# Kernel optimization log

Hardware: AMD Instinct MI355X
Metric: run time of the kernel (lower is better)

## Reference

```python
import jax, jax.numpy as jnp
import numpy as np

B, N, H, NH = 8, 1024, 768, 12
AS = H // NH
SCALE = AS ** -0.5
NEG_SLOPE = 0.02  # LeakyReLU(0.02)
M = 256           # occurrence pairs per batch item


def _lin(k, out_d, in_d):
    k1, k2 = jax.random.split(k)
    w = jax.random.normal(k1, (out_d, in_d), jnp.float32) * (in_d ** -0.5)
    b = jax.random.normal(k2, (out_d,), jnp.float32) * 0.01
    return w, b


def setup_inputs():
    key = jax.random.key(0)
    ks = jax.random.split(key, 10)
    W_var, b_var = _lin(ks[0], H, H)
    W_sym, b_sym = _lin(ks[1], H, H)
    W_score, b_score = _lin(ks[2], 1, 2 * H)
    W_cross, b_cross = _lin(ks[3], 1, H)
    W_atom, b_atom = _lin(ks[4], H, 2 * H)
    W_q, b_q = _lin(ks[5], H, H)
    W_k, b_k = _lin(ks[6], H, H)
    W_v, b_v = _lin(ks[7], H, H)
    W_o, b_o = _lin(ks[8], H, H)
    x = jax.random.normal(ks[9], (B, N, H), jnp.float32)
    # predicates every 3rd node starting at 2 (no overlapping writes, i+1 < N)
    pp = np.zeros((B, N), np.int32)
    pp[:, 2:N - 2:3] = 1
    rng = np.random.default_rng(0)
    occ = np.stack([rng.permutation(N)[:2 * M].reshape(M, 2) for _ in range(B)]).astype(np.int32)
    return dict(
        x=x,
        atom_graph=jnp.zeros((B, N, N), jnp.float32),
        variable_graph=jnp.zeros((B, N, N), jnp.float32),
        W_var=W_var, b_var=b_var, W_sym=W_sym, b_sym=b_sym,
        W_score=W_score, b_score=b_score, W_cross=W_cross, b_cross=b_cross,
        W_atom=W_atom, b_atom=b_atom, W_q=W_q, b_q=b_q, W_k=W_k, b_k=b_k,
        W_v=W_v, b_v=b_v, W_o=W_o, b_o=b_o,
        predicate_pos=jnp.asarray(pp),
        variable_tags=jnp.zeros((B, N), jnp.int32),
        attention_mask=jnp.ones((B, N), jnp.int32),
        occurrence_list=jnp.asarray(occ),
    )


def reference(x, atom_graph, variable_graph,
              W_var, b_var, W_sym, b_sym, W_score, b_score, W_cross, b_cross,
              W_atom, b_atom, W_q, b_q, W_k, b_k, W_v, b_v, W_o, b_o,
              predicate_pos, variable_tags, attention_mask, occurrence_list):
    lrelu = lambda v: jax.nn.leaky_relu(v, NEG_SLOPE)
    idx = jnp.arange(N)
    pred = predicate_pos == 1                              # [B,N]
    pp_prev2 = jnp.roll(predicate_pos, 2, axis=1)          # pp[i-2]
    # branch: single-neighbor var (i==0 or pp[i-2]==1) vs averaged neighbors
    single = (idx[None, :] == 0) | ((idx[None, :] >= 2) & (pp_prev2 == 1))
    x_prev = jnp.roll(x, 1, axis=1)
    x_next = jnp.roll(x, -1, axis=1)
    var_in = jnp.where(single[..., None], x_next, (x_prev + x_next) * 0.5)
    var_feat = var_in @ W_var.T + b_var
    sym_feat = x @ W_sym.T + b_sym
    t = jnp.tanh(jnp.concatenate([var_feat, sym_feat], axis=-1))
    s = lrelu(t @ W_score.T + b_score)[..., 0]             # [B,N] edge scores
    # write masks: (i-1,i)/(i,i-1) for preds i>=1; (i,i+1)/(i+1,i) for i<=1 or double branch
    lower = pred & (idx[None, :] >= 1)
    upper = pred & ((idx[None, :] <= 1) | ~single)
    sl = jnp.where(lower, s, 0.0)
    su = jnp.where(upper, s, 0.0)
    im1 = jnp.clip(idx - 1, 0, N - 1)
    ip1 = jnp.clip(idx + 1, 0, N - 1)
    AG = atom_graph
    AG = AG.at[:, im1, idx].add(sl).at[:, idx, im1].add(sl)
    AG = AG.at[:, idx, ip1].add(su).at[:, ip1, idx].add(su)
    # variable (cross-atom occurrence) graph
    o0, o1 = occurrence_list[..., 0], occurrence_list[..., 1]
    barange = jnp.arange(B)[:, None]
    xm = (x[barange, o0] + x[barange, o1]) * 0.5           # [B,M,H]
    sc = lrelu(xm @ W_cross.T + b_cross)[..., 0]           # [B,M]
    VG = variable_graph.at[barange, o0, o1].add(sc).at[barange, o1, o0].add(sc)
    # multi-head attention with graph biases
    q = (x @ W_q.T + b_q).reshape(B, N, NH, AS).transpose(0, 2, 1, 3) * SCALE
    k = (x @ W_k.T + b_k).reshape(B, N, NH, AS).transpose(0, 2, 1, 3)
    v = (x @ W_v.T + b_v).reshape(B, N, NH, AS).transpose(0, 2, 1, 3)
    att = jnp.einsum('bhnd,bhmd->bhnm', q, k)
    AG = 0.2 * AG + 0.8 * (AG @ AG)
    VG2 = VG @ VG
    att = att + AG[:, None] + VG2[:, None]
    att = jax.nn.softmax(att, axis=-1)                     # dropout omitted (eval)
    y = jnp.einsum('bhnm,bhmd->bhnd', att, v).transpose(0, 2, 1, 3).reshape(B, N, H)
    y = y @ W_o.T + b_o
    # path embedding: weighted mean of per-predicate atom embeds (weight 2 or 3)
    y_prev = jnp.roll(y, 1, axis=1)
    y_next = jnp.roll(y, -1, axis=1)
    var_y = jnp.where(single[..., None], y_next, (y_prev + y_next) * 0.5)
    atom = jnp.concatenate([var_y, y], axis=-1) @ W_atom.T + b_atom  # [B,N,H]
    triple = upper & (idx[None, :] >= 1)
    w = jnp.where(pred, jnp.where(triple, 3.0, 2.0), 0.0)
    pm = (w[..., None] * atom).sum(axis=1) / w.sum(axis=1)[:, None]  # [B,H]
    return jnp.broadcast_to(pm[:, None, :], (B, N, H))
```

## Files before the change

kernel.cpp:

```cpp
#include <hip/hip_runtime.h>
#include <hip/hip_bf16.h>

#define BB 8
#define NN 1024
#define HH 768
#define NHD 12
#define ASZ 64
#define MM 256
#define QSCALE 0.125f
#define NSLOPE 0.02f
#define LOG2E 1.44269504f
#define PRMAX 384

typedef __attribute__((ext_vector_type(8))) short bf16x8;
typedef __attribute__((ext_vector_type(4))) float f32x4;

#define EXP2F(x) __builtin_amdgcn_exp2f(x)
#define RCPF(x)  __builtin_amdgcn_rcpf(x)

#define OFFB_QB    ((size_t)0)
#define OFFB_KB    ((size_t)12582912)
#define OFFB_VB    ((size_t)25165824)
#define OFFB_XB    ((size_t)37748736)
#define OFFB_WQB   ((size_t)50331648)
// ... 72 lines not shown
  if (lane == 0) { pcnt[b] = base; sumw[b] = wacc; }
  for (int c = lane; c < NN; c += 64) { sraw[b * NN + c] = 0.f; diag[b * NN + c] = 0.f; }
  for (int c = lane; c < HH; c += 64) {
    zz[b * HH + c] = 0.f;
    zz[BB * HH + b * HH + c] = 0.f;
  }
}

#define NXQ (BB * NN * HH / 4)
#define WQ  (HH * HH / 4)
#define NCVT ((NXQ + 5 * WQ) / 256)
__global__ void k_cvtall(const float* __restrict__ x,
                         const float* __restrict__ s1, const float* __restrict__ s2,
                         const float* __restrict__ s3, const float* __restrict__ s4,
                         const float* __restrict__ s5,
                         ushort* __restrict__ dx,
                         ushort* __restrict__ d1, ushort* __restrict__ d2,
                         ushort* __restrict__ d3, ushort* __restrict__ d4,
                         ushort* __restrict__ d5,
                         const int* __restrict__ occ, const float* __restrict__ Wc,
                         const float* __restrict__ bc, float* __restrict__ diag) {
  if (blockIdx.x < NCVT) {
    int idx = blockIdx.x * 256 + threadIdx.x;
    const float* src; ushort* dst; int off;
    if (idx < NXQ) { src = x; dst = dx; off = idx; }
    else {
      int r = idx - NXQ;
      int z = r / WQ;
      off = r - z * WQ;
      src = z == 0 ? s1 : z == 1 ? s2 : z == 2 ? s3 : z == 3 ? s4 : s5;
      dst = z == 0 ? d1 : z == 1 ? d2 : z == 2 ? d3 : z == 3 ? d4 : d5;
    }
    float4 v = ((const float4*)src)[off];
    ushort4 o;
    o.x = f2bf(v.x); o.y = f2bf(v.y); o.z = f2bf(v.z); o.w = f2bf(v.w);
    ((ushort4*)dst)[off] = o;
  } else {
    int g = (blockIdx.x - NCVT) * 4 + (threadIdx.x >> 6);
    int lane = threadIdx.x & 63;
    int b = g >> 8, m = g & (MM - 1);
    int o0 = occ[(b * MM + m) * 2 + 0];
    int o1 = occ[(b * MM + m) * 2 + 1];
    const float* x0 = x + (size_t)(b * NN + o0) * HH;
    const float* x1 = x + (size_t)(b * NN + o1) * HH;
    float acc = 0.f;
    for (int d = lane; d < HH; d += 64) acc += 0.5f * (x0[d] + x1[d]) * Wc[d];
    for (int off = 32; off; off >>= 1) acc += __shfl_xor(acc, off);
    if (lane == 0) {
      float sc = lrelu(acc + bc[0]);
      float sq = sc * sc;
      diag[b * NN + o0] = sq;
      diag[b * NN + o1] = sq;
    }
  }
}

__global__ void k_gather(const ushort* __restrict__ xb, const int* __restrict__ pp,
                         const int* __restrict__ plist, const int* __restrict__ pcnt,
                         ushort* __restrict__ vrows) {
  int b = blockIdx.y;
  int j = blockIdx.x * 4 + (threadIdx.x >> 6);
  int lane = threadIdx.x & 63;
  if (j >= pcnt[b]) return;
  int i = plist[b * NN + j];
  bool sing = (i == 0) || (i >= 2 && pp[b * NN + i - 2] == 1);
  float wa = sing ? 0.f : 0.5f, wb = sing ? 1.f : 0.5f;
  const ushort* rp = xb + (size_t)(b * NN + ((i - 1) & (NN - 1))) * HH;
  const ushort* rn = xb + (size_t)(b * NN + ((i + 1) & (NN - 1))) * HH;
  ushort* dst = vrows + ((size_t)b * PRMAX + j) * HH;
#pragma unroll
  for (int it = 0; it < 3; ++it) {
    int d4 = lane + it * 64;
    ushort4 p4 = ((const ushort4*)rp)[d4];
    ushort4 n4 = ((const ushort4*)rn)[d4];
    ushort4 o;
    o.x = f2bf(wa * bf2f(p4.x) + wb * bf2f(n4.x));
    o.y = f2bf(wa * bf2f(p4.y) + wb * bf2f(n4.y));
    o.z = f2bf(wa * bf2f(p4.z) + wb * bf2f(n4.z));
    o.w = f2bf(wa * bf2f(p4.w) + wb * bf2f(n4.w));
    ((ushort4*)dst)[d4] = o;
  }
}

__global__ __launch_bounds__(256, 2) void k_score_mf(
    const ushort* __restrict__ xb, const ushort* __restrict__ vrows,
    const int* __restrict__ plist, const int* __restrict__ pcnt,
    const ushort* __restrict__ Wvar, const ushort* __restrict__ Wsym,
    const float* __restrict__ bvar, const float* __restrict__ bsym,
    const float* __restrict__ wscore, float* __restrict__ s_raw) {
  const int b = blockIdx.z;
  const int cnt = pcnt[b];
  const int j0 = blockIdx.y * 64;
  if (j0 >= cnt) return;
  const int n0g = blockIdx.x * 128;
  const bool symh = n0g >= HH;
  const int n0 = symh ? n0g - HH : n0g;
  const ushort* W = symh ? Wsym : Wvar;
  const float* bias = symh ? bsym : bvar;
  __shared__ ushort As[64 * 64];
  __shared__ ushort Bs[128 * 64];
  __shared__ int pl[64];
  __shared__ float red[64];
  const int t = threadIdx.x;
  const int w = t >> 6, lane = t & 63, lg = lane >> 4, lm = lane & 15;
  const int wm = (w >> 1) * 32, wn = (w & 1) * 64;
  if (t < 64) {
    int j = j0 + t;
    pl[t] = (j < cnt) ? plist[b * NN + j] : 2;
    red[t] = 0.f;
  }
  __syncthreads();
  const int r0 = t >> 3, c = t & 7;
  const ushort* ap0; const ushort* ap1;
  if (symh) {
    const ushort* xbb = xb + (size_t)b * NN * HH;
    ap0 = xbb + (size_t)pl[r0] * HH + c * 8;
    ap1 = xbb + (size_t)pl[r0 + 32] * HH + c * 8;
  } else {
    const ushort* vrb = vrows + ((size_t)b * PRMAX + j0) * HH;
    ap0 = vrb + (size_t)r0 * HH + c * 8;
    ap1 = vrb + (size_t)(r0 + 32) * HH + c * 8;
  }
  const ushort* bp = W + (size_t)(n0 + r0) * HH + c * 8;
  uint4 ar0 = *(const uint4*)ap0;
  uint4 ar1 = *(const uint4*)ap1;
  uint4 br0 = *(const uint4*)bp;
  uint4 br1 = *(const uint4*)(bp + (size_t)32 * HH);
  uint4 br2 = *(const uint4*)(bp + (size_t)64 * HH);
  uint4 br3 = *(const uint4*)(bp + (size_t)96 * HH);
  f32x4 acc[2][4] = {};
  const int ssw = (c ^ (r0 & 7)) * 8;
  for (int k0 = 0; k0 < HH; k0 += 64) {
    if (k0) __syncthreads();
    *(uint4*)&As[r0 * 64 + ssw] = ar0;
    *(uint4*)&As[(r0 + 32) * 64 + ssw] = ar1;
    *(uint4*)&Bs[r0 * 64 + ssw] = br0;
    *(uint4*)&Bs[(r0 + 32) * 64 + ssw] = br1;
    *(uint4*)&Bs[(r0 + 64) * 64 + ssw] = br2;
    *(uint4*)&Bs[(r0 + 96) * 64 + ssw] = br3;
    __syncthreads();
    if (k0 + 64 < HH) {
      ap0 += 64; ap1 += 64; bp += 64;
      ar0 = *(const uint4*)ap0;
      ar1 = *(const uint4*)ap1;
      br0 = *(const uint4*)bp;
      br1 = *(const uint4*)(bp + (size_t)32 * HH);
      br2 = *(const uint4*)(bp + (size_t)64 * HH);
      br3 = *(const uint4*)(bp + (size_t)96 * HH);
    }
    bf16x8 af[2][2], bfr[4][2];
#pragma unroll
    for (int mt = 0; mt < 2; ++mt)
#pragma unroll
      for (int kt = 0; kt < 2; ++kt) {
        int row = wm + mt * 16 + lm, ch = lg + kt * 4;
        af[mt][kt] = *(bf16x8*)&As[row * 64 + ((ch ^ (row & 7)) * 8)];
      }
#pragma unroll
    for (int nt = 0; nt < 4; ++nt)
#pragma unroll
      for (int kt = 0; kt < 2; ++kt) {
        int row = wn + nt * 16 + lm, ch = lg + kt * 4;
        bfr[nt][kt] = *(bf16x8*)&Bs[row * 64 + ((ch ^ (row & 7)) * 8)];
      }
#pragma unroll
    for (int mt = 0; mt < 2; ++mt)
#pragma unroll
      for (int nt = 0; nt < 4; ++nt)
#pragma unroll
        for (int kt = 0; kt < 2; ++kt)
          acc[mt][nt] = __builtin_amdgcn_mfma_f32_16x16x32_bf16(af[mt][kt], bfr[nt][kt], acc[mt][nt], 0, 0, 0);
  }
  float bcol[4], wcol[4];
#pragma unroll
  for (int nt = 0; nt < 4; ++nt) {
    int cl = wn + nt * 16 + lm;
    bcol[nt] = bias[n0 + cl];
    wcol[nt] = wscore[n0g + cl];
  }
#pragma unroll
  for (int mt = 0; mt < 2; ++mt)
#pragma unroll
    for (int r = 0; r < 4; ++r) {
      float p = 0.f;
#pragma unroll
      for (int nt = 0; nt < 4; ++nt)
        p += fast_tanh(acc[mt][nt][r] + bcol[nt]) * wcol[nt];
      p += __shfl_xor(p, 1); p += __shfl_xor(p, 2);
      p += __shfl_xor(p, 4); p += __shfl_xor(p, 8);
      if (lm == 0) atomicAdd(&red[wm + mt * 16 + lg * 4 + r], p);
    }
  __syncthreads();
  if (t < 64) {
    int j2 = j0 + t;
    if (j2 < cnt) atomicAdd(&s_raw[b * NN + pl[t]], red[t]);
  }
}

__global__ void k_bias(const int* __restrict__ pp, const float* __restrict__ s_raw,
                       const float* __restrict__ diag, const float* __restrict__ b_score,
                       float4* __restrict__ bias4) {
  int g = blockIdx.x * 256 + threadIdx.x;
  int b = g >> 10, r = g & (NN - 1);
  const int* ppb = pp + b * NN;
  int i = -1;
  if (ppb[r] == 1) i = r;
  else if (r + 1 < NN && ppb[r + 1] == 1) i = r + 1;
  else if (r >= 1 && ppb[r - 1] == 1) i = r - 1;
  float v0 = 0.f, v1 = 0.f, v2 = 0.f; int cw = r;
  if (i >= 1 && i + 1 < NN) {
    float s = lrelu(s_raw[b * NN + i] + b_score[0]);
    float s2 = s * s;
    cw = i - 1;
    if (i == r) { v0 = 0.2f * s; v1 = 1.6f * s2; v2 = 0.2f * s; }
    else       { v0 = 0.8f * s2; v1 = 0.2f * s; v2 = 0.8f * s2; }
  }
  int slot = r - cw;
  float d = diag[g];
  if (slot == 0) v0 += d; else if (slot == 1) v1 += d; else v2 += d;
  bias4[g] = make_float4(__int_as_float(cw), v0 * LOG2E, v1 * LOG2E, v2 * LOG2E);
}

__global__ __launch_bounds__(256, 2) void k_gemm_bf(
    const ushort* __restrict__ X,
    const ushort* __restrict__ W0, const ushort* __restrict__ W1, const ushort* __restrict__ W2,
    const float* __restrict__ b0, const float* __restrict__ b1, const float* __restrict__ b2,
    ushort* __restrict__ C0, ushort* __restrict__ C1, ushort* __restrict__ C2) {
  const int z = blockIdx.z;
  const ushort* W = z == 0 ? W0 : (z == 1 ? W1 : W2);
  const float* bias = z == 0 ? b0 : (z == 1 ? b1 : b2);
  ushort* C = z == 0 ? C0 : (z == 1 ? C1 : C2);
  const float alpha = z == 0 ? QSCALE * LOG2E : 1.f;
  __shared__ ushort As[128 * 64];
  __shared__ ushort Bs[128 * 64];
  const int m0 = blockIdx.x * 128, n0 = blockIdx.y * 128;
  const int t = threadIdx.x;
  const int w = t >> 6, lane = t & 63, lg = lane >> 4, lm = lane & 15;
  const int wm = (w >> 1) * 64, wn = (w & 1) * 64;
  const int r0 = t >> 3, c = t & 7;
  const int ssw = (c ^ (r0 & 7)) * 8;
  const ushort* Xp = X + (size_t)(m0 + r0) * HH + c * 8;
  const ushort* Wp = W + (size_t)(n0 + r0) * HH + c * 8;
  uint4 xa0 = *(const uint4*)Xp;
  uint4 xa1 = *(const uint4*)(Xp + (size_t)32 * HH);
  uint4 xa2 = *(const uint4*)(Xp + (size_t)64 * HH);
  uint4 xa3 = *(const uint4*)(Xp + (size_t)96 * HH);
  uint4 wb0 = *(const uint4*)Wp;
  uint4 wb1 = *(const uint4*)(Wp + (size_t)32 * HH);
  uint4 wb2 = *(const uint4*)(Wp + (size_t)64 * HH);
  uint4 wb3 = *(const uint4*)(Wp + (size_t)96 * HH);
  f32x4 acc[4][4] = {};
  for (int k0 = 0; k0 < HH; k0 += 64) {
    if (k0) __syncthreads();
    *(uint4*)&As[r0 * 64 + ssw] = xa0;
    *(uint4*)&As[(r0 + 32) * 64 + ssw] = xa1;
    *(uint4*)&As[(r0 + 64) * 64 + ssw] = xa2;
    *(uint4*)&As[(r0 + 96) * 64 + ssw] = xa3;
    *(uint4*)&Bs[r0 * 64 + ssw] = wb0;
    *(uint4*)&Bs[(r0 + 32) * 64 + ssw] = wb1;
    *(uint4*)&Bs[(r0 + 64) * 64 + ssw] = wb2;
    *(uint4*)&Bs[(r0 + 96) * 64 + ssw] = wb3;
    __syncthreads();
    if (k0 + 64 < HH) {
      Xp += 64; Wp += 64;
      xa0 = *(const uint4*)Xp;
      xa1 = *(const uint4*)(Xp + (size_t)32 * HH);
      xa2 = *(const uint4*)(Xp + (size_t)64 * HH);
      xa3 = *(const uint4*)(Xp + (size_t)96 * HH);
      wb0 = *(const uint4*)Wp;
      wb1 = *(const uint4*)(Wp + (size_t)32 * HH);
      wb2 = *(const uint4*)(Wp + (size_t)64 * HH);
      wb3 = *(const uint4*)(Wp + (size_t)96 * HH);
    }
    bf16x8 af[4][2], bfr[4][2];
#pragma unroll
    for (int mt = 0; mt < 4; ++mt)
#pragma unroll
      for (int kt = 0; kt < 2; ++kt) {
        int row = wm + mt * 16 + lm, ch = lg + kt * 4;
        af[mt][kt] = *(bf16x8*)&As[row * 64 + ((ch ^ (row & 7)) * 8)];
      }
#pragma unroll
    for (int nt = 0; nt < 4; ++nt)
#pragma unroll
      for (int kt = 0; kt < 2; ++kt) {
        int row = wn + nt * 16 + lm, ch = lg + kt * 4;
        bfr[nt][kt] = *(bf16x8*)&Bs[row * 64 + ((ch ^ (row & 7)) * 8)];
      }
#pragma unroll
    for (int mt = 0; mt < 4; ++mt)
#pragma unroll
      for (int nt = 0; nt < 4; ++nt)
#pragma unroll
        for (int kt = 0; kt < 2; ++kt)
          acc[mt][nt] = __builtin_amdgcn_mfma_f32_16x16x32_bf16(af[mt][kt], bfr[nt][kt], acc[mt][nt], 0, 0, 0);
  }
  if (z == 2) {
#pragma unroll
    for (int nt = 0; nt < 4; ++nt) {
      int col = n0 + wn + nt * 16 + lm;
      int hh = col >> 6, dd = col & 63;
      float bcol = bias[col];
#pragma unroll
      for (int mt = 0; mt < 4; ++mt) {
        int row0 = m0 + wm + mt * 16 + lg * 4;
        int bb2 = row0 >> 10, nr = row0 & (NN - 1);
        ushort4 o;
        o.x = f2bf(acc[mt][nt][0] + bcol);
        o.y = f2bf(acc[mt][nt][1] + bcol);
        o.z = f2bf(acc[mt][nt][2] + bcol);
        o.w = f2bf(acc[mt][nt][3] + bcol);
        *(ushort4*)(C + ((size_t)(bb2 * NHD + hh) * ASZ + dd) * NN + nr) = o;
      }
    }
  } else {
#pragma unroll
    for (int nt = 0; nt < 4; ++nt) {
      int col = n0 + wn + nt * 16 + lm;
      float bcol = bias[col];
#pragma unroll
      for (int mt = 0; mt < 4; ++mt)
#pragma unroll
        for (int r = 0; r < 4; ++r) {
          int row = m0 + wm + mt * 16 + lg * 4 + r;
          C[(size_t)row * HH + col] = f2bf((acc[mt][nt][r] + bcol) * alpha);
        }
    }
  }
}

__global__ __launch_bounds__(512, 2) void k_attn2(
    const ushort* __restrict__ qg, const ushort* __restrict__ kg, const ushort* __restrict__ vtg,
    const float4* __restrict__ bias4, const int* __restrict__ pp, float* __restrict__ zz) {
  __shared__ ushort Ks[128 * 64];
  __shared__ ushort Vts[64 * 128];
  const int rb = blockIdx.y, h = blockIdx.x >> 3, b = blockIdx.x & 7;
  const int n0 = rb * 128;
  const int t = threadIdx.x, w = t >> 6, lane = t & 63, lg = lane >> 4, lm = lane & 15;
  const int qbase = n0 + w * 16;
  const ushort* qrow = qg + (size_t)(b * NN + qbase + lm) * HH + h * ASZ;
  bf16x8 qf[2];
  qf[0] = *(const bf16x8*)(qrow + lg * 8);
  qf[1] = *(const bf16x8*)(qrow + lg * 8 + 32);
  float4 bz = bias4[b * NN + qbase + lm];
  const int cwq = __float_as_int(bz.x);
  float mr = -1e30f, lr = 0.f;
  f32x4 y[4] = {};
  const ushort* kb = kg + (size_t)(b * NN) * HH + h * ASZ;
  const ushort* vtb = vtg + (size_t)(b * NHD + h) * ASZ * NN;
  const int srow = t >> 3, sc = t & 7;
  const int arow = (srow & 35) | ((srow & 4) << 2) | ((srow & 24) >> 1);
  const int kssw = (sc ^ (arow & 7)) * 8;
  const int vd = t >> 4, vc = t & 15;
  const int vssw = (vc ^ ((vd & 7) << 1)) * 8;
  const ushort* kptr = kb + (size_t)srow * HH + sc * 8;
  const ushort* vptr = vtb + (size_t)vd * NN + vc * 8;
  uint4 ka = *(const uint4*)kptr;
  uint4 kc = *(const uint4*)(kptr + (size_t)64 * HH);
  uint4 va = *(const uint4*)vptr;
  uint4 vb2 = *(const uint4*)(vptr + (size_t)32 * NN);
  for (int tile = 0; tile < 8; ++tile) {
    const int c0 = tile * 128;
    *(uint4*)&Ks[arow * 64 + kssw] = ka;
    *(uint4*)&Ks[(arow + 64) * 64 + kssw] = kc;
    *(uint4*)&Vts[vd * 128 + vssw] = va;
    *(uint4*)&Vts[(vd + 32) * 128 + vssw] = vb2;
    __syncthreads();
    if (tile < 7) {
      kptr += (size_t)128 * HH; vptr += 128;
      ka = *(const uint4*)kptr;
      kc = *(const uint4*)(kptr + (size_t)64 * HH);
      va = *(const uint4*)vptr;
      vb2 = *(const uint4*)(vptr + (size_t)32 * NN);
    }
    f32x4 s[8] = {};
    __builtin_amdgcn_s_setprio(1);
#pragma unroll
    for (int nt = 0; nt < 8; ++nt) {
      int krow = lm + nt * 16, sw = krow & 7;
#pragma unroll
      for (int kt = 0; kt < 2; ++kt) {
        bf16x8 kf = *(bf16x8*)&Ks[krow * 64 + (((lg + kt * 4) ^ sw) * 8)];
        s[nt] = __builtin_amdgcn_mfma_f32_16x16x32_bf16(kf, qf[kt], s[nt], 0, 0, 0);
      }
    }
    __builtin_amdgcn_s_setprio(0);
    if (c0 <= qbase + 17 && qbase <= c0 + 129) {
#pragma unroll
      for (int nt = 0; nt < 8; ++nt) {
        int kb2 = c0 + (nt >> 1) * 32 + lg * 8 + (nt & 1) * 4;
#pragma unroll
        for (int r = 0; r < 4; ++r) {
          int dd = kb2 + r - cwq;
          if (dd >= 0 && dd < 3) s[nt][r] += (dd == 0) ? bz.y : (dd == 1 ? bz.z : bz.w);
        }
      }
    }
    f32x4 mA, mB;
#pragma unroll
    for (int e = 0; e < 4; ++e) {
      mA[e] = fmaxf(fmaxf(s[0][e], s[1][e]), fmaxf(s[2][e], s[3][e]));
      mB[e] = fmaxf(fmaxf(s[4][e], s[5][e]), fmaxf(s[6][e], s[7][e]));
      mA[e] = fmaxf(mA[e], mB[e]);
    }
    float tm = fmaxf(fmaxf(mA[0], mA[1]), fmaxf(mA[2], mA[3]));
    tm = fmaxf(tm, __shfl_xor(tm, 16));
    tm = fmaxf(tm, __shfl_xor(tm, 32));
    int need = tm > mr;
    if (__any(need)) {
      float mn = fmaxf(mr, tm);
      float f = EXP2F(mr - mn);
      mr = mn;
      lr *= f;
      float fr[4];
#pragma unroll
      for (int r = 0; r < 4; ++r) fr[r] = __shfl(f, lg * 4 + r);
#pragma unroll
      for (int nt = 0; nt < 4; ++nt)
#pragma unroll
        for (int r = 0; r < 4; ++r) y[nt][r] *= fr[r];
    }
    f32x4 sum4 = {0.f, 0.f, 0.f, 0.f};
#pragma unroll
    for (int nt = 0; nt < 8; ++nt)
#pragma unroll
      for (int e = 0; e < 4; ++e) {
        float p = EXP2F(s[nt][e] - mr);
        s[nt][e] = p;
        sum4[e] += p;
      }
    float ts = (sum4[0] + sum4[1]) + (sum4[2] + sum4[3]);
    ts += __shfl_xor(ts, 16);
    ts += __shfl_xor(ts, 32);
    lr += ts;
    union { unsigned u[4]; bf16x8 v; } pk[4];
#pragma unroll
    for (int kt = 0; kt < 4; ++kt) {
      pk[kt].u[0] = packbf2(s[2 * kt][0], s[2 * kt][1]);
      pk[kt].u[1] = packbf2(s[2 * kt][2], s[2 * kt][3]);
      pk[kt].u[2] = packbf2(s[2 * kt + 1][0], s[2 * kt + 1][1]);
      pk[kt].u[3] = packbf2(s[2 * kt + 1][2], s[2 * kt + 1][3]);
    }
    __builtin_amdgcn_s_setprio(1);
#pragma unroll
    for (int nt = 0; nt < 4; ++nt) {
      int vrow = lm + nt * 16, sw2 = (vrow & 7) << 1;
#pragma unroll
      for (int kt = 0; kt < 4; ++kt) {
        bf16x8 vf = *(bf16x8*)&Vts[vrow * 128 + (((kt * 4 + lg) ^ sw2) * 8)];
        y[nt] = __builtin_amdgcn_mfma_f32_16x16x32_bf16(pk[kt].v, vf, y[nt], 0, 0, 0);
      }
    }
    __builtin_amdgcn_s_setprio(0);
    __syncthreads();
  }
  float invl = 1.f / lr;
  float invq[4], c1v[4], c2v[4];
#pragma unroll
  for (int r = 0; r < 4; ++r) {
    invq[r] = __shfl(invl, lg * 4 + r);
    coefs(pp + b * NN, qbase + lg * 4 + r, c1v[r], c2v[r]);
  }
  float a1[4], a2[4];
#pragma unroll
  for (int nt = 0; nt < 4; ++nt) {
    float u1 = 0.f, u2 = 0.f;
#pragma unroll
    for (int r = 0; r < 4; ++r) {
      float yv = y[nt][r] * invq[r];
      u1 += c1v[r] * yv;
      u2 += c2v[r] * yv;
    }
    u1 += __shfl_xor(u1, 16); u1 += __shfl_xor(u1, 32);
    u2 += __shfl_xor(u2, 16); u2 += __shfl_xor(u2, 32);
    a1[nt] = u1; a2[nt] = u2;
  }
  if (lg == 0) {
#pragma unroll
    for (int nt = 0; nt < 4; ++nt) {
      atomicAdd(&zz[b * HH + h * ASZ + nt * 16 + lm], a1[nt]);
      atomicAdd(&zz[BB * HH + b * HH + h * ASZ + nt * 16 + lm], a2[nt]);
    }
  }
}

__global__ void k_f1(const float* __restrict__ Wo, const float* __restrict__ bo,
                     const float* __restrict__ zz, const float* __restrict__ sumw,
                     float* __restrict__ tvec) {
  int b = blockIdx.y;
  int w = threadIdx.x >> 6, lane = threadIdx.x & 63;
  float inv = 1.f / sumw[b];
  const float* z1 = zz + b * HH;
  const float* z2 = zz + BB * HH + b * HH;
  float zr1[12], zr2[12];
#pragma unroll
  for (int m = 0; m < 12; ++m) { zr1[m] = z1[lane + 64 * m] * inv; zr2[m] = z2[lane + 64 * m] * inv; }
  for (int j = 0; j < 8; ++j) {
    int o = blockIdx.x * 32 + w * 8 + j;
    const float* wrow = Wo + (size_t)o * HH;
    float a1 = 0.f, a2 = 0.f;
#pragma unroll
    for (int m = 0; m < 12; ++m) { float wv = wrow[lane + 64 * m]; a1 += wv * zr1[m]; a2 += wv * zr2[m]; }
    for (int mask = 32; mask; mask >>= 1) { a1 += __shfl_xor(a1, mask); a2 += __shfl_xor(a2, mask); }
    if (lane == 0) { tvec[b * HH + o] = a1 + bo[o]; tvec[BB * HH + b * HH + o] = a2 + bo[o]; }
  }
}

__global__ void k_f2(const float* __restrict__ Wa, const float* __restrict__ ba,
                     const float* __restrict__ tvec, float* __restrict__ pm) {
  int b = blockIdx.y;
  int w = threadIdx.x >> 6, lane = threadIdx.x & 63;
  const float* t1 = tvec + b * HH;
  const float* t2 = tvec + BB * HH + b * HH;
  float r1[12], r2[12];
#pragma unroll
  for (int m = 0; m < 12; ++m) { r1[m] = t1[lane + 64 * m]; r2[m] = t2[lane + 64 * m]; }
  for (int j = 0; j < 8; ++j) {
    int o = blockIdx.x * 32 + w * 8 + j;
    const float* wrow = Wa + (size_t)o * (2 * HH);
    float a = 0.f;
#pragma unroll
    for (int m = 0; m < 12; ++m) a += wrow[lane + 64 * m] * r1[m];
#pragma unroll
    for (int m = 0; m < 12; ++m) a += wrow[HH + lane + 64 * m] * r2[m];
    for (int mask = 32; mask; mask >>= 1) a += __shfl_xor(a, mask);
    if (lane == 0) pm[b * HH + o] = a + ba[o];
  }
}

__global__ void k_bcast(const float* __restrict__ pm, float* __restrict__ out) {
  size_t g = (size_t)blockIdx.x * 256 + threadIdx.x;
  int b = (int)(g / ((size_t)NN * HH / 4));
  int hh4 = (int)(g % (HH / 4));
  float4 val = *(const float4*)(pm + b * HH + hh4 * 4);
  *(float4*)(out + g * 4) = val;
}

extern "C" void kernel_launch(void* const* d_in, const int* in_sizes, int n_in,
                              void* d_out, int out_size, void* d_ws, size_t ws_size,
                              hipStream_t stream) {
  (void)in_sizes; (void)n_in; (void)out_size; (void)ws_size;
  const float* x       = (const float*)d_in[0];
  const float* W_var   = (const float*)d_in[3];
  const float* b_var   = (const float*)d_in[4];
  const float* W_sym   = (const float*)d_in[5];
  const float* b_sym   = (const float*)d_in[6];
  const float* W_score = (const float*)d_in[7];
  const float* b_score = (const float*)d_in[8];
  const float* W_cross = (const float*)d_in[9];
  const float* b_cross = (const float*)d_in[10];
  const float* W_atom  = (const float*)d_in[11];
  const float* b_atom  = (const float*)d_in[12];
  const float* W_q     = (const float*)d_in[13];
  const float* b_q     = (const float*)d_in[14];
  const float* W_k     = (const float*)d_in[15];
  const float* b_k     = (const float*)d_in[16];
  const float* W_v     = (const float*)d_in[17];
  const float* b_v     = (const float*)d_in[18];
  const float* W_o     = (const float*)d_in[19];
  const float* b_o     = (const float*)d_in[20];
  const int*   pp      = (const int*)d_in[21];
  const int*   occ     = (const int*)d_in[24];
  float* out = (float*)d_out;
  char* wsb = (char*)d_ws;
  ushort* qb  = (ushort*)(wsb + OFFB_QB);
  ushort* kbf = (ushort*)(wsb + OFFB_KB);
  ushort* vtb = (ushort*)(wsb + OFFB_VB);
  ushort* xb  = (ushort*)(wsb + OFFB_XB);
  ushort* wqb = (ushort*)(wsb + OFFB_WQB);
  ushort* wkb = (ushort*)(wsb + OFFB_WKB);
  ushort* wvb = (ushort*)(wsb + OFFB_WVB);
  ushort* wvar = (ushort*)(wsb + OFFB_WVAR);
  ushort* wsym = (ushort*)(wsb + OFFB_WSYM);
  ushort* vrows = (ushort*)(wsb + OFFB_VROWS);
  float* sraw = (float*)(wsb + OFFB_SRAW);
  float* diag = (float*)(wsb + OFFB_DIAG);
  float4* bias4 = (float4*)(wsb + OFFB_BIAS4);
  int* plist = (int*)(wsb + OFFB_PLIST);
  int* pcnt  = (int*)(wsb + OFFB_PCNT);
  float* sumw = (float*)(wsb + OFFB_SUMW);
  float* zz   = (float*)(wsb + OFFB_ZZ);
  float* tv   = (float*)(wsb + OFFB_TV);
  float* pm   = (float*)(wsb + OFFB_PM);

  k_pred<<<BB, 64, 0, stream>>>(pp, plist, pcnt, sumw, sraw, diag, zz);
  k_cvtall<<<NCVT + BB * MM / 4, 256, 0, stream>>>(
      x, W_q, W_k, W_v, W_var, W_sym, xb, wqb, wkb, wvb, wvar, wsym,
      occ, W_cross, b_cross, diag);
  k_gather<<<dim3(PRMAX / 4, BB), 256, 0, stream>>>(xb, pp, plist, pcnt, vrows);
  k_score_mf<<<dim3(12, 6, BB), 256, 0, stream>>>(xb, vrows, plist, pcnt, wvar, wsym,
                                                  b_var, b_sym, W_score, sraw);
  k_bias<<<BB * NN / 256, 256, 0, stream>>>(pp, sraw, diag, b_score, bias4);
  k_gemm_bf<<<dim3(64, 6, 3), 256, 0, stream>>>(xb, wqb, wkb, wvb, b_q, b_k, b_v, qb, kbf, vtb);
  k_attn2<<<dim3(NHD * BB, NN / 128), 512, 0, stream>>>(qb, kbf, vtb, bias4, pp, zz);
  k_f1<<<dim3(24, BB), 256, 0, stream>>>(W_o, b_o, zz, sumw, tv);
  k_f2<<<dim3(24, BB), 256, 0, stream>>>(W_atom, b_atom, tv, pm);
  k_bcast<<<BB * NN * HH / 1024, 256, 0, stream>>>(pm, out);
}
```

Measured before the change: 162.3 us.

## Merge score and QKV GEMMs into one launch; shrink attention tiles to 64

The score GEMM and the QKV projection GEMM are combined into a single kernel launch, with the block index choosing which work each block does. This removes a launch and lets the small score GEMM overlap with the large QKV GEMM. The attention kernel moves from 128-row, 512-thread blocks with 128-key tiles to 64-row, 256-thread blocks with 64-key tiles and a higher occupancy bound. That doubles the grid and the number of tile iterations, trading more loop overhead and synchronisation for better occupancy and load balance.

```diff
diff --git a/kernel.cpp b/kernel.cpp
--- a/kernel.cpp
+++ b/kernel.cpp
@@ -178,121 +178,6 @@
   }
 }
 
-__global__ __launch_bounds__(256, 2) void k_score_mf(
-    const ushort* __restrict__ xb, const ushort* __restrict__ vrows,
-    const int* __restrict__ plist, const int* __restrict__ pcnt,
-    const ushort* __restrict__ Wvar, const ushort* __restrict__ Wsym,
-    const float* __restrict__ bvar, const float* __restrict__ bsym,
-    const float* __restrict__ wscore, float* __restrict__ s_raw) {
-  const int b = blockIdx.z;
-  const int cnt = pcnt[b];
-  const int j0 = blockIdx.y * 64;
-  if (j0 >= cnt) return;
-  const int n0g = blockIdx.x * 128;
-  const bool symh = n0g >= HH;
-  const int n0 = symh ? n0g - HH : n0g;
-  const ushort* W = symh ? Wsym : Wvar;
-  const float* bias = symh ? bsym : bvar;
-  __shared__ ushort As[64 * 64];
-  __shared__ ushort Bs[128 * 64];
-  __shared__ int pl[64];
-  __shared__ float red[64];
-  const int t = threadIdx.x;
-  const int w = t >> 6, lane = t & 63, lg = lane >> 4, lm = lane & 15;
-  const int wm = (w >> 1) * 32, wn = (w & 1) * 64;
-  if (t < 64) {
-    int j = j0 + t;
-    pl[t] = (j < cnt) ? plist[b * NN + j] : 2;
-    red[t] = 0.f;
-  }
-  __syncthreads();
-  const int r0 = t >> 3, c = t & 7;
-  const ushort* ap0; const ushort* ap1;
-  if (symh) {
-    const ushort* xbb = xb + (size_t)b * NN * HH;
-    ap0 = xbb + (size_t)pl[r0] * HH + c * 8;
-    ap1 = xbb + (size_t)pl[r0 + 32] * HH + c * 8;
-  } else {
-    const ushort* vrb = vrows + ((size_t)b * PRMAX + j0) * HH;
-    ap0 = vrb + (size_t)r0 * HH + c * 8;
-    ap1 = vrb + (size_t)(r0 + 32) * HH + c * 8;
-  }
-  const ushort* bp = W + (size_t)(n0 + r0) * HH + c * 8;
-  uint4 ar0 = *(const uint4*)ap0;
-  uint4 ar1 = *(const uint4*)ap1;
-  uint4 br0 = *(const uint4*)bp;
-  uint4 br1 = *(const uint4*)(bp + (size_t)32 * HH);
-  uint4 br2 = *(const uint4*)(bp + (size_t)64 * HH);
-  uint4 br3 = *(const uint4*)(bp + (size_t)96 * HH);
-  f32x4 acc[2][4] = {};
-  const int ssw = (c ^ (r0 & 7)) * 8;
-  for (int k0 = 0; k0 < HH; k0 += 64) {
-    if (k0) __syncthreads();
-    *(uint4*)&As[r0 * 64 + ssw] = ar0;
-    *(uint4*)&As[(r0 + 32) * 64 + ssw] = ar1;
-    *(uint4*)&Bs[r0 * 64 + ssw] = br0;
-    *(uint4*)&Bs[(r0 + 32) * 64 + ssw] = br1;
-    *(uint4*)&Bs[(r0 + 64) * 64 + ssw] = br2;
-    *(uint4*)&Bs[(r0 + 96) * 64 + ssw] = br3;
-    __syncthreads();
-    if (k0 + 64 < HH) {
-      ap0 += 64; ap1 += 64; bp += 64;
-      ar0 = *(const uint4*)ap0;
-      ar1 = *(const uint4*)ap1;
-      br0 = *(const uint4*)bp;
-      br1 = *(const uint4*)(bp + (size_t)32 * HH);
-      br2 = *(const uint4*)(bp + (size_t)64 * HH);
-      br3 = *(const uint4*)(bp + (size_t)96 * HH);
-    }
-    bf16x8 af[2][2], bfr[4][2];
-#pragma unroll
-    for (int mt = 0; mt < 2; ++mt)
-#pragma unroll
-      for (int kt = 0; kt < 2; ++kt) {
-        int row = wm + mt * 16 + lm, ch = lg + kt * 4;
-        af[mt][kt] = *(bf16x8*)&As[row * 64 + ((ch ^ (row & 7)) * 8)];
-      }
-#pragma unroll
-    for (int nt = 0; nt < 4; ++nt)
-#pragma unroll
-      for (int kt = 0; kt < 2; ++kt) {
-        int row = wn + nt * 16 + lm, ch = lg + kt * 4;
-        bfr[nt][kt] = *(bf16x8*)&Bs[row * 64 + ((ch ^ (row & 7)) * 8)];
-      }
-#pragma unroll
-    for (int mt = 0; mt < 2; ++mt)
-#pragma unroll
-      for (int nt = 0; nt < 4; ++nt)
-#pragma unroll
-        for (int kt = 0; kt < 2; ++kt)
-          acc[mt][nt] = __builtin_amdgcn_mfma_f32_16x16x32_bf16(af[mt][kt], bfr[nt][kt], acc[mt][nt], 0, 0, 0);
-  }
-  float bcol[4], wcol[4];
-#pragma unroll
-  for (int nt = 0; nt < 4; ++nt) {
-    int cl = wn + nt * 16 + lm;
-    bcol[nt] = bias[n0 + cl];
-    wcol[nt] = wscore[n0g + cl];
-  }
-#pragma unroll
-  for (int mt = 0; mt < 2; ++mt)
-#pragma unroll
-    for (int r = 0; r < 4; ++r) {
-      float p = 0.f;
-#pragma unroll
-      for (int nt = 0; nt < 4; ++nt)
-        p += fast_tanh(acc[mt][nt][r] + bcol[nt]) * wcol[nt];
-      p += __shfl_xor(p, 1); p += __shfl_xor(p, 2);
-      p += __shfl_xor(p, 4); p += __shfl_xor(p, 8);
-      if (lm == 0) atomicAdd(&red[wm + mt * 16 + lg * 4 + r], p);
-    }
-  __syncthreads();
-  if (t < 64) {
-    int j2 = j0 + t;
-    if (j2 < cnt) atomicAdd(&s_raw[b * NN + pl[t]], red[t]);
-  }
-}
-
 __global__ void k_bias(const int* __restrict__ pp, const float* __restrict__ s_raw,
                        const float* __restrict__ diag, const float* __restrict__ b_score,
                        float4* __restrict__ bias4) {
@@ -317,121 +202,236 @@
   bias4[g] = make_float4(__int_as_float(cw), v0 * LOG2E, v1 * LOG2E, v2 * LOG2E);
 }
 
-__global__ __launch_bounds__(256, 2) void k_gemm_bf(
-    const ushort* __restrict__ X,
+#define GEMM_BLKS 1152
+__global__ __launch_bounds__(256, 2) void k_mats(
+    const ushort* __restrict__ X, const ushort* __restrict__ vrows,
+    const int* __restrict__ plist, const int* __restrict__ pcnt,
+    const ushort* __restrict__ Wvar, const ushort* __restrict__ Wsym,
+    const float* __restrict__ bvar, const float* __restrict__ bsym,
+    const float* __restrict__ wscore, float* __restrict__ s_raw,
     const ushort* __restrict__ W0, const ushort* __restrict__ W1, const ushort* __restrict__ W2,
     const float* __restrict__ b0, const float* __restrict__ b1, const float* __restrict__ b2,
     ushort* __restrict__ C0, ushort* __restrict__ C1, ushort* __restrict__ C2) {
-  const int z = blockIdx.z;
-  const ushort* W = z == 0 ? W0 : (z == 1 ? W1 : W2);
-  const float* bias = z == 0 ? b0 : (z == 1 ? b1 : b2);
-  ushort* C = z == 0 ? C0 : (z == 1 ? C1 : C2);
-  const float alpha = z == 0 ? QSCALE * LOG2E : 1.f;
-  __shared__ ushort As[128 * 64];
-  __shared__ ushort Bs[128 * 64];
-  const int m0 = blockIdx.x * 128, n0 = blockIdx.y * 128;
+  __shared__ ushort Sm[16384];
+  __shared__ int pl[64];
+  __shared__ float red[64];
   const int t = threadIdx.x;
   const int w = t >> 6, lane = t & 63, lg = lane >> 4, lm = lane & 15;
-  const int wm = (w >> 1) * 64, wn = (w & 1) * 64;
   const int r0 = t >> 3, c = t & 7;
   const int ssw = (c ^ (r0 & 7)) * 8;
-  const ushort* Xp = X + (size_t)(m0 + r0) * HH + c * 8;
-  const ushort* Wp = W + (size_t)(n0 + r0) * HH + c * 8;
-  uint4 xa0 = *(const uint4*)Xp;
-  uint4 xa1 = *(const uint4*)(Xp + (size_t)32 * HH);
-  uint4 xa2 = *(const uint4*)(Xp + (size_t)64 * HH);
-  uint4 xa3 = *(const uint4*)(Xp + (size_t)96 * HH);
-  uint4 wb0 = *(const uint4*)Wp;
-  uint4 wb1 = *(const uint4*)(Wp + (size_t)32 * HH);
-  uint4 wb2 = *(const uint4*)(Wp + (size_t)64 * HH);
-  uint4 wb3 = *(const uint4*)(Wp + (size_t)96 * HH);
-  f32x4 acc[4][4] = {};
-  for (int k0 = 0; k0 < HH; k0 += 64) {
-    if (k0) __syncthreads();
-    *(uint4*)&As[r0 * 64 + ssw] = xa0;
-    *(uint4*)&As[(r0 + 32) * 64 + ssw] = xa1;
-    *(uint4*)&As[(r0 + 64) * 64 + ssw] = xa2;
-    *(uint4*)&As[(r0 + 96) * 64 + ssw] = xa3;
-    *(uint4*)&Bs[r0 * 64 + ssw] = wb0;
-    *(uint4*)&Bs[(r0 + 32) * 64 + ssw] = wb1;
-    *(uint4*)&Bs[(r0 + 64) * 64 + ssw] = wb2;
-    *(uint4*)&Bs[(r0 + 96) * 64 + ssw] = wb3;
+  if (blockIdx.x < GEMM_BLKS) {
+    const int z = blockIdx.x / 384;
+    const int r = blockIdx.x % 384;
+    const int m0 = (r & 63) * 128, n0 = (r >> 6) * 128;
+    const ushort* W = z == 0 ? W0 : (z == 1 ? W1 : W2);
+    const float* bias = z == 0 ? b0 : (z == 1 ? b1 : b2);
+    ushort* C = z == 0 ? C0 : (z == 1 ? C1 : C2);
+    const float alpha = z == 0 ? QSCALE * LOG2E : 1.f;
+    ushort* As = Sm;
+    ushort* Bs = Sm + 8192;
+    const int wm = (w >> 1) * 64, wn = (w & 1) * 64;
+    const ushort* Xp = X + (size_t)(m0 + r0) * HH + c * 8;
+    const ushort* Wp = W + (size_t)(n0 + r0) * HH + c * 8;
+    uint4 xa0 = *(const uint4*)Xp;
+    uint4 xa1 = *(const uint4*)(Xp + (size_t)32 * HH);
+    uint4 xa2 = *(const uint4*)(Xp + (size_t)64 * HH);
+    uint4 xa3 = *(const uint4*)(Xp + (size_t)96 * HH);
+    uint4 wb0 = *(const uint4*)Wp;
+    uint4 wb1 = *(const uint4*)(Wp + (size_t)32 * HH);
+    uint4 wb2 = *(const uint4*)(Wp + (size_t)64 * HH);
+    uint4 wb3 = *(const uint4*)(Wp + (size_t)96 * HH);
+    f32x4 acc[4][4] = {};
+    for (int k0 = 0; k0 < HH; k0 += 64) {
+      if (k0) __syncthreads();
+      *(uint4*)&As[r0 * 64 + ssw] = xa0;
+      *(uint4*)&As[(r0 + 32) * 64 + ssw] = xa1;
+      *(uint4*)&As[(r0 + 64) * 64 + ssw] = xa2;
+      *(uint4*)&As[(r0 + 96) * 64 + ssw] = xa3;
+      *(uint4*)&Bs[r0 * 64 + ssw] = wb0;
+      *(uint4*)&Bs[(r0 + 32) * 64 + ssw] = wb1;
+      *(uint4*)&Bs[(r0 + 64) * 64 + ssw] = wb2;
+      *(uint4*)&Bs[(r0 + 96) * 64 + ssw] = wb3;
+      __syncthreads();
+      if (k0 + 64 < HH) {
+        Xp += 64; Wp += 64;
+        xa0 = *(const uint4*)Xp;
+        xa1 = *(const uint4*)(Xp + (size_t)32 * HH);
+        xa2 = *(const uint4*)(Xp + (size_t)64 * HH);
+        xa3 = *(const uint4*)(Xp + (size_t)96 * HH);
+        wb0 = *(const uint4*)Wp;
+        wb1 = *(const uint4*)(Wp + (size_t)32 * HH);
+        wb2 = *(const uint4*)(Wp + (size_t)64 * HH);
+        wb3 = *(const uint4*)(Wp + (size_t)96 * HH);
+      }
+      bf16x8 af[4][2], bfr[4][2];
+#pragma unroll
+      for (int mt = 0; mt < 4; ++mt)
+#pragma unroll
+        for (int kt = 0; kt < 2; ++kt) {
+          int row = wm + mt * 16 + lm, ch = lg + kt * 4;
+          af[mt][kt] = *(bf16x8*)&As[row * 64 + ((ch ^ (row & 7)) * 8)];
+        }
+#pragma unroll
+      for (int nt = 0; nt < 4; ++nt)
+#pragma unroll
+        for (int kt = 0; kt < 2; ++kt) {
+          int row = wn + nt * 16 + lm, ch = lg + kt * 4;
+          bfr[nt][kt] = *(bf16x8*)&Bs[row * 64 + ((ch ^ (row & 7)) * 8)];
+        }
+#pragma unroll
+      for (int mt = 0; mt < 4; ++mt)
+#pragma unroll
+        for (int nt = 0; nt < 4; ++nt)
+#pragma unroll
+          for (int kt = 0; kt < 2; ++kt)
+            acc[mt][nt] = __builtin_amdgcn_mfma_f32_16x16x32_bf16(af[mt][kt], bfr[nt][kt], acc[mt][nt], 0, 0, 0);
+    }
+    if (z == 2) {
+#pragma unroll
+      for (int nt = 0; nt < 4; ++nt) {
+        int col = n0 + wn + nt * 16 + lm;
+        int hh = col >> 6, dd = col & 63;
+        float bcol = bias[col];
+#pragma unroll
+        for (int mt = 0; mt < 4; ++mt) {
+          int row0 = m0 + wm + mt * 16 + lg * 4;
+          int bb2 = row0 >> 10, nr = row0 & (NN - 1);
+          ushort4 o;
+          o.x = f2bf(acc[mt][nt][0] + bcol);
+          o.y = f2bf(acc[mt][nt][1] + bcol);
+          o.z = f2bf(acc[mt][nt][2] + bcol);
+          o.w = f2bf(acc[mt][nt][3] + bcol);
+          *(ushort4*)(C + ((size_t)(bb2 * NHD + hh) * ASZ + dd) * NN + nr) = o;
+        }
+      }
+    } else {
+#pragma unroll
+      for (int nt = 0; nt < 4; ++nt) {
+        int col = n0 + wn + nt * 16 + lm;
+        float bcol = bias[col];
+#pragma unroll
+        for (int mt = 0; mt < 4; ++mt)
+#pragma unroll
+          for (int rr = 0; rr < 4; ++rr) {
+            int row = m0 + wm + mt * 16 + lg * 4 + rr;
+            C[(size_t)row * HH + col] = f2bf((acc[mt][nt][rr] + bcol) * alpha);
+          }
+      }
+    }
+  } else {
+    const int bid2 = blockIdx.x - GEMM_BLKS;
+    const int b = bid2 / 72;
+    const int rem = bid2 % 72;
+    const int j0 = (rem / 12) * 64;
+    const int n0g = (rem % 12) * 128;
+    const int cnt = pcnt[b];
+    if (j0 >= cnt) return;
+    const bool symh = n0g >= HH;
+    const int n0 = symh ? n0g - HH : n0g;
+    const ushort* W = symh ? Wsym : Wvar;
+    const float* bias = symh ? bsym : bvar;
+    ushort* As = Sm;
+    ushort* Bs = Sm + 4096;
+    const int wm = (w >> 1) * 32, wn = (w & 1) * 64;
+    if (t < 64) {
+      int j = j0 + t;
+      pl[t] = (j < cnt) ? plist[b * NN + j] : 2;
+      red[t] = 0.f;
+    }
     __syncthreads();
-    if (k0 + 64 < HH) {
-      Xp += 64; Wp += 64;
-      xa0 = *(const uint4*)Xp;
-      xa1 = *(const uint4*)(Xp + (size_t)32 * HH);
-      xa2 = *(const uint4*)(Xp + (size_t)64 * HH);
-      xa3 = *(const uint4*)(Xp + (size_t)96 * HH);
-      wb0 = *(const uint4*)Wp;
-      wb1 = *(const uint4*)(Wp + (size_t)32 * HH);
-      wb2 = *(const uint4*)(Wp + (size_t)64 * HH);
-      wb3 = *(const uint4*)(Wp + (size_t)96 * HH);
-    }
-    bf16x8 af[4][2], bfr[4][2];
-#pragma unroll
-    for (int mt = 0; mt < 4; ++mt)
-#pragma unroll
-      for (int kt = 0; kt < 2; ++kt) {
-        int row = wm + mt * 16 + lm, ch = lg + kt * 4;
-        af[mt][kt] = *(bf16x8*)&As[row * 64 + ((ch ^ (row & 7)) * 8)];
-      }
-#pragma unroll
-    for (int nt = 0; nt < 4; ++nt)
-#pragma unroll
-      for (int kt = 0; kt < 2; ++kt) {
-        int row = wn + nt * 16 + lm, ch = lg + kt * 4;
-        bfr[nt][kt] = *(bf16x8*)&Bs[row * 64 + ((ch ^ (row & 7)) * 8)];
-      }
-#pragma unroll
-    for (int mt = 0; mt < 4; ++mt)
+    const ushort* ap0; const ushort* ap1;
+    if (symh) {
+      const ushort* xbb = X + (size_t)b * NN * HH;
+      ap0 = xbb + (size_t)pl[r0] * HH + c * 8;
+      ap1 = xbb + (size_t)pl[r0 + 32] * HH + c * 8;
+    } else {
+      const ushort* vrb = vrows + ((size_t)b * PRMAX + j0) * HH;
+      ap0 = vrb + (size_t)r0 * HH + c * 8;
+      ap1 = vrb + (size_t)(r0 + 32) * HH + c * 8;
+    }
+    const ushort* bp = W + (size_t)(n0 + r0) * HH + c * 8;
+    uint4 ar0 = *(const uint4*)ap0;
+    uint4 ar1 = *(const uint4*)ap1;
+    uint4 br0 = *(const uint4*)bp;
+    uint4 br1 = *(const uint4*)(bp + (size_t)32 * HH);
+    uint4 br2 = *(const uint4*)(bp + (size_t)64 * HH);
+    uint4 br3 = *(const uint4*)(bp + (size_t)96 * HH);
+    f32x4 acc[2][4] = {};
+    for (int k0 = 0; k0 < HH; k0 += 64) {
+      if (k0) __syncthreads();
+      *(uint4*)&As[r0 * 64 + ssw] = ar0;
+      *(uint4*)&As[(r0 + 32) * 64 + ssw] = ar1;
+      *(uint4*)&Bs[r0 * 64 + ssw] = br0;
+      *(uint4*)&Bs[(r0 + 32) * 64 + ssw] = br1;
+      *(uint4*)&Bs[(r0 + 64) * 64 + ssw] = br2;
+      *(uint4*)&Bs[(r0 + 96) * 64 + ssw] = br3;
+      __syncthreads();
+      if (k0 + 64 < HH) {
+        ap0 += 64; ap1 += 64; bp += 64;
+        ar0 = *(const uint4*)ap0;
+        ar1 = *(const uint4*)ap1;
+        br0 = *(const uint4*)bp;
+        br1 = *(const uint4*)(bp + (size_t)32 * HH);
+        br2 = *(const uint4*)(bp + (size_t)64 * HH);
+        br3 = *(const uint4*)(bp + (size_t)96 * HH);
+      }
+      bf16x8 af[2][2], bfr[4][2];
+#pragma unroll
+      for (int mt = 0; mt < 2; ++mt)
+#pragma unroll
+        for (int kt = 0; kt < 2; ++kt) {
+          int row = wm + mt * 16 + lm, ch = lg + kt * 4;
+          af[mt][kt] = *(bf16x8*)&As[row * 64 + ((ch ^ (row & 7)) * 8)];
+        }
 #pragma unroll
       for (int nt = 0; nt < 4; ++nt)
 #pragma unroll
-        for (int kt = 0; kt < 2; ++kt)
-          acc[mt][nt] = __builtin_amdgcn_mfma_f32_16x16x32_bf16(af[mt][kt], bfr[nt][kt], acc[mt][nt], 0, 0, 0);
-  }
-  if (z == 2) {
+        for (int kt = 0; kt < 2; ++kt) {
+          int row = wn + nt * 16 + lm, ch = lg + kt * 4;
+          bfr[nt][kt] = *(bf16x8*)&Bs[row * 64 + ((ch ^ (row & 7)) * 8)];
+        }
+#pragma unroll
+      for (int mt = 0; mt < 2; ++mt)
+#pragma unroll
+        for (int nt = 0; nt < 4; ++nt)
+#pragma unroll
+          for (int kt = 0; kt < 2; ++kt)
+            acc[mt][nt] = __builtin_amdgcn_mfma_f32_16x16x32_bf16(af[mt][kt], bfr[nt][kt], acc[mt][nt], 0, 0, 0);
+    }
+    float bcol[4], wcol[4];
 #pragma unroll
     for (int nt = 0; nt < 4; ++nt) {
-      int col = n0 + wn + nt * 16 + lm;
-      int hh = col >> 6, dd = col & 63;
-      float bcol = bias[col];
-#pragma unroll
-      for (int mt = 0; mt < 4; ++mt) {
-        int row0 = m0 + wm + mt * 16 + lg * 4;
-        int bb2 = row0 >> 10, nr = row0 & (NN - 1);
-        ushort4 o;
-        o.x = f2bf(acc[mt][nt][0] + bcol);
-        o.y = f2bf(acc[mt][nt][1] + bcol);
-        o.z = f2bf(acc[mt][nt][2] + bcol);
-        o.w = f2bf(acc[mt][nt][3] + bcol);
-        *(ushort4*)(C + ((size_t)(bb2 * NHD + hh) * ASZ + dd) * NN + nr) = o;
-      }
-    }
-  } else {
-#pragma unroll
-    for (int nt = 0; nt < 4; ++nt) {
-      int col = n0 + wn + nt * 16 + lm;
-      float bcol = bias[col];
-#pragma unroll
-      for (int mt = 0; mt < 4; ++mt)
-#pragma unroll
-        for (int r = 0; r < 4; ++r) {
-          int row = m0 + wm + mt * 16 + lg * 4 + r;
-          C[(size_t)row * HH + col] = f2bf((acc[mt][nt][r] + bcol) * alpha);
-        }
-    }
-  }
-}
-
-__global__ __launch_bounds__(512, 2) void k_attn2(
+      int cl = wn + nt * 16 + lm;
+      bcol[nt] = bias[n0 + cl];
+      wcol[nt] = wscore[n0g + cl];
+    }
+#pragma unroll
+    for (int mt = 0; mt < 2; ++mt)
+#pragma unroll
+      for (int rr = 0; rr < 4; ++rr) {
+        float p = 0.f;
+#pragma unroll
+        for (int nt = 0; nt < 4; ++nt)
+          p += fast_tanh(acc[mt][nt][rr] + bcol[nt]) * wcol[nt];
+        p += __shfl_xor(p, 1); p += __shfl_xor(p, 2);
+        p += __shfl_xor(p, 4); p += __shfl_xor(p, 8);
+        if (lm == 0) atomicAdd(&red[wm + mt * 16 + lg * 4 + rr], p);
+      }
+    __syncthreads();
+    if (t < 64) {
+      int j2 = j0 + t;
+      if (j2 < cnt) atomicAdd(&s_raw[b * NN + pl[t]], red[t]);
+    }
+  }
+}
+
+__global__ __launch_bounds__(256, 4) void k_attn2(
     const ushort* __restrict__ qg, const ushort* __restrict__ kg, const ushort* __restrict__ vtg,
     const float4* __restrict__ bias4, const int* __restrict__ pp, float* __restrict__ zz) {
-  __shared__ ushort Ks[128 * 64];
-  __shared__ ushort Vts[64 * 128];
+  __shared__ ushort Ks[64 * 64];
+  __shared__ ushort Vts[64 * 64];
   const int rb = blockIdx.y, h = blockIdx.x >> 3, b = blockIdx.x & 7;
-  const int n0 = rb * 128;
+  const int n0 = rb * 64;
   const int t = threadIdx.x, w = t >> 6, lane = t & 63, lg = lane >> 4, lm = lane & 15;
   const int qbase = n0 + w * 16;
   const ushort* qrow = qg + (size_t)(b * NN + qbase + lm) * HH + h * ASZ;
@@ -447,32 +447,31 @@
   const int srow = t >> 3, sc = t & 7;
   const int arow = (srow & 35) | ((srow & 4) << 2) | ((srow & 24) >> 1);
   const int kssw = (sc ^ (arow & 7)) * 8;
-  const int vd = t >> 4, vc = t & 15;
-  const int vssw = (vc ^ ((vd & 7) << 1)) * 8;
+  const int vssw = (sc ^ (srow & 7)) * 8;
   const ushort* kptr = kb + (size_t)srow * HH + sc * 8;
-  const ushort* vptr = vtb + (size_t)vd * NN + vc * 8;
+  const ushort* vptr = vtb + (size_t)srow * NN + sc * 8;
   uint4 ka = *(const uint4*)kptr;
-  uint4 kc = *(const uint4*)(kptr + (size_t)64 * HH);
+  uint4 kc = *(const uint4*)(kptr + (size_t)32 * HH);
   uint4 va = *(const uint4*)vptr;
   uint4 vb2 = *(const uint4*)(vptr + (size_t)32 * NN);
-  for (int tile = 0; tile < 8; ++tile) {
-    const int c0 = tile * 128;
+  for (int tile = 0; tile < 16; ++tile) {
+    const int c0 = tile * 64;
     *(uint4*)&Ks[arow * 64 + kssw] = ka;
-    *(uint4*)&Ks[(arow + 64) * 64 + kssw] = kc;
-    *(uint4*)&Vts[vd * 128 + vssw] = va;
-    *(uint4*)&Vts[(vd + 32) * 128 + vssw] = vb2;
+    *(uint4*)&Ks[(arow + 32) * 64 + kssw] = kc;
+    *(uint4*)&Vts[srow * 64 + vssw] = va;
+    *(uint4*)&Vts[(srow + 32) * 64 + vssw] = vb2;
     __syncthreads();
-    if (tile < 7) {
-      kptr += (size_t)128 * HH; vptr += 128;
+    if (tile < 15) {
+      kptr += (size_t)64 * HH; vptr += 64;
       ka = *(const uint4*)kptr;
-      kc = *(const uint4*)(kptr + (size_t)64 * HH);
+      kc = *(const uint4*)(kptr + (size_t)32 * HH);
       va = *(const uint4*)vptr;
       vb2 = *(const uint4*)(vptr + (size_t)32 * NN);
     }
-    f32x4 s[8] = {};
+    f32x4 s[4] = {};
     __builtin_amdgcn_s_setprio(1);
 #pragma unroll
-    for (int nt = 0; nt < 8; ++nt) {
+    for (int nt = 0; nt < 4; ++nt) {
       int krow = lm + nt * 16, sw = krow & 7;
 #pragma unroll
       for (int kt = 0; kt < 2; ++kt) {
@@ -481,9 +480,9 @@
       }
     }
     __builtin_amdgcn_s_setprio(0);
-    if (c0 <= qbase + 17 && qbase <= c0 + 129) {
-#pragma unroll
-      for (int nt = 0; nt < 8; ++nt) {
+    if (c0 <= qbase + 17 && qbase <= c0 + 65) {
+#pragma unroll
+      for (int nt = 0; nt < 4; ++nt) {
         int kb2 = c0 + (nt >> 1) * 32 + lg * 8 + (nt & 1) * 4;
 #pragma unroll
         for (int r = 0; r < 4; ++r) {
@@ -492,14 +491,11 @@
         }
       }
     }
-    f32x4 mA, mB;
-#pragma unroll
-    for (int e = 0; e < 4; ++e) {
-      mA[e] = fmaxf(fmaxf(s[0][e], s[1][e]), fmaxf(s[2][e], s[3][e]));
-      mB[e] = fmaxf(fmaxf(s[4][e], s[5][e]), fmaxf(s[6][e], s[7][e]));
-      mA[e] = fmaxf(mA[e], mB[e]);
-    }
-    float tm = fmaxf(fmaxf(mA[0], mA[1]), fmaxf(mA[2], mA[3]));
+    f32x4 m4;
+#pragma unroll
+    for (int e = 0; e < 4; ++e)
+      m4[e] = fmaxf(fmaxf(s[0][e], s[1][e]), fmaxf(s[2][e], s[3][e]));
+    float tm = fmaxf(fmaxf(m4[0], m4[1]), fmaxf(m4[2], m4[3]));
     tm = fmaxf(tm, __shfl_xor(tm, 16));
     tm = fmaxf(tm, __shfl_xor(tm, 32));
     int need = tm > mr;
@@ -518,7 +514,7 @@
     }
     f32x4 sum4 = {0.f, 0.f, 0.f, 0.f};
 #pragma unroll
-    for (int nt = 0; nt < 8; ++nt)
+    for (int nt = 0; nt < 4; ++nt)
 #pragma unroll
       for (int e = 0; e < 4; ++e) {
         float p = EXP2F(s[nt][e] - mr);
@@ -529,9 +525,9 @@
     ts += __shfl_xor(ts, 16);
     ts += __shfl_xor(ts, 32);
     lr += ts;
-    union { unsigned u[4]; bf16x8 v; } pk[4];
-#pragma unroll
-    for (int kt = 0; kt < 4; ++kt) {
+    union { unsigned u[4]; bf16x8 v; } pk[2];
+#pragma unroll
+    for (int kt = 0; kt < 2; ++kt) {
       pk[kt].u[0] = packbf2(s[2 * kt][0], s[2 * kt][1]);
       pk[kt].u[1] = packbf2(s[2 * kt][2], s[2 * kt][3]);
       pk[kt].u[2] = packbf2(s[2 * kt + 1][0], s[2 * kt + 1][1]);
@@ -540,10 +536,10 @@
     __builtin_amdgcn_s_setprio(1);
 #pragma unroll
     for (int nt = 0; nt < 4; ++nt) {
-      int vrow = lm + nt * 16, sw2 = (vrow & 7) << 1;
-#pragma unroll
-      for (int kt = 0; kt < 4; ++kt) {
-        bf16x8 vf = *(bf16x8*)&Vts[vrow * 128 + (((kt * 4 + lg) ^ sw2) * 8)];
+      int vrow = lm + nt * 16, sw = vrow & 7;
+#pragma unroll
+      for (int kt = 0; kt < 2; ++kt) {
+        bf16x8 vf = *(bf16x8*)&Vts[vrow * 64 + (((lg + kt * 4) ^ sw) * 8)];
         y[nt] = __builtin_amdgcn_mfma_f32_16x16x32_bf16(pk[kt].v, vf, y[nt], 0, 0, 0);
       }
     }
@@ -684,11 +680,11 @@
       x, W_q, W_k, W_v, W_var, W_sym, xb, wqb, wkb, wvb, wvar, wsym,
       occ, W_cross, b_cross, diag);
   k_gather<<<dim3(PRMAX / 4, BB), 256, 0, stream>>>(xb, pp, plist, pcnt, vrows);
-  k_score_mf<<<dim3(12, 6, BB), 256, 0, stream>>>(xb, vrows, plist, pcnt, wvar, wsym,
-                                                  b_var, b_sym, W_score, sraw);
+  k_mats<<<GEMM_BLKS + 576, 256, 0, stream>>>(
+      xb, vrows, plist, pcnt, wvar, wsym, b_var, b_sym, W_score, sraw,
+      wqb, wkb, wvb, b_q, b_k, b_v, qb, kbf, vtb);
   k_bias<<<BB * NN / 256, 256, 0, stream>>>(pp, sraw, diag, b_score, bias4);
-  k_gemm_bf<<<dim3(64, 6, 3), 256, 0, stream>>>(xb, wqb, wkb, wvb, b_q, b_k, b_v, qb, kbf, vtb);
-  k_attn2<<<dim3(NHD * BB, NN / 128), 512, 0, stream>>>(qb, kbf, vtb, bias4, pp, zz);
+  k_attn2<<<dim3(NHD * BB, NN / 64), 256, 0, stream>>>(qb, kbf, vtb, bias4, pp, zz);
   k_f1<<<dim3(24, BB), 256, 0, stream>>>(W_o, b_o, zz, sumw, tv);
   k_f2<<<dim3(24, BB), 256, 0, stream>>>(W_atom, b_atom, tv, pm);
   k_bcast<<<BB * NN * HH / 1024, 256, 0, stream>>>(pm, out);
```

Measured after the change: 157.9 us. 2.7% less time.
